# Kernel optimization log

Hardware: AMD Instinct MI355X
Metric: run time of the kernel (lower is better)

The kernel has to match this reference:

```python
import jax, jax.numpy as jnp
import numpy as np

N_NODES = 100000
N_EDGES = 800000
IN_DIM, HID, OUT_DIM = 128, 96, 32
BN_EPS = 1e-5


def gcn_conv(x, W, b, src, dst, n):
    # PyG GCNConv: linear -> symmetric-normalized aggregation (with self-loops) -> +bias
    h = x @ W  # [N, out]
    sl = jnp.arange(n)
    s = jnp.concatenate([src, sl])
    d = jnp.concatenate([dst, sl])
    deg = jax.ops.segment_sum(jnp.ones(s.shape[0], dtype=x.dtype), d, num_segments=n)
    dinv = jnp.where(deg > 0, jax.lax.rsqrt(deg), 0.0)
    norm = dinv[s] * dinv[d]  # [E+N]
    out = jax.ops.segment_sum(norm[:, None] * h[s], d, num_segments=n)
    return out + b


def batchnorm(x, gamma, beta):
    mu = jnp.mean(x, axis=0)
    var = jnp.var(x, axis=0)
    return gamma * (x - mu) * jax.lax.rsqrt(var + BN_EPS) + beta


def setup_inputs() -> dict:
    key = jax.random.key(0)
    ks = jax.random.split(key, 8)
    glorot = lambda k, fi, fo: jax.random.normal(k, (fi, fo), jnp.float32) * np.sqrt(2.0 / (fi + fo))
    return {
        "x": jax.random.normal(ks[0], (N_NODES, IN_DIM), jnp.float32),
        "edge_index": jax.random.randint(ks[1], (2, N_EDGES), 0, N_NODES, jnp.int64),
        "W1": glorot(ks[2], IN_DIM, HID), "b1": jnp.zeros((HID,), jnp.float32),
        "W2": glorot(ks[3], HID, HID), "b2": jnp.zeros((HID,), jnp.float32),
        "W3": glorot(ks[4], HID, OUT_DIM), "b3": jnp.zeros((OUT_DIM,), jnp.float32),
        "g1": jnp.ones((HID,), jnp.float32), "be1": jnp.zeros((HID,), jnp.float32),
        "g2": jnp.ones((HID,), jnp.float32), "be2": jnp.zeros((HID,), jnp.float32),
    }


def reference(x, edge_index, W1, b1, W2, b2, W3, b3, g1, be1, g2, be2):
    src, dst = edge_index[0], edge_index[1]
    n = x.shape[0]
    h = gcn_conv(x, W1, b1, src, dst, n)
    h = jax.nn.relu(batchnorm(h, g1, be1))  # dropout is identity in eval
    h = gcn_conv(h, W2, b2, src, dst, n)
    h = jax.nn.relu(batchnorm(h, g2, be2))
    h = gcn_conv(h, W3, b3, src, dst, n)
    return jax.nn.log_softmax(h, axis=-1)
```

## Files before the change

kernel.cpp:

```cpp
#include <hip/hip_runtime.h>
#include <hip/hip_fp16.h>
#include <cstddef>

#define NN 100000
#define NE 800000
#define DIN 128
#define HID 96
#define DOUT 32
static constexpr float BN_EPS = 1e-5f;
#define SCAN_NB ((NN + 255) / 256)

typedef unsigned short u16;
typedef unsigned int u32;

__device__ __forceinline__ float b2f(u32 lo16) {
    union { u32 u; float f; } c; c.u = lo16 << 16; return c.f;
}
__device__ __forceinline__ u16 f2b(float f) {
    union { float f; u32 u; } c; c.f = f;
    return (u16)((c.u + 0x7FFFu + ((c.u >> 16) & 1u)) >> 16);
}
__device__ __forceinline__ u32 pack_edge(int s, float w) {
    __half h = __float2half(w);
    return ((u32)s << 15) | (u32)__half_as_ushort(h);
}
__device__ __forceinline__ int edge_src(u32 pk) { return (int)(pk >> 15); }
__device__ __forceinline__ float edge_wt(u32 pk) {
    return __half2float(__ushort_as_half((u16)(pk & 0x7FFFu)));
}


__global__ void k_init(int* __restrict__ deg) {
    int i = blockIdx.x * 256 + threadIdx.x;
    if (i < NN) deg[i] = 0;
}

__global__ __launch_bounds__(256) void k_scan1(const int* __restrict__ deg,
                                               int* __restrict__ row_start,
                                               int* __restrict__ blksum,
                                               float* __restrict__ dinv) {
    __shared__ int lds[256];
    int t = threadIdx.x;
    int i = blockIdx.x * 256 + t;
    int v = (i < NN) ? deg[i] : 0;
    if (i < NN) dinv[i] = rsqrtf((float)(v + 1));
    lds[t] = v;
    __syncthreads();
#pragma unroll
    for (int off = 1; off < 256; off <<= 1) {
        int add = (t >= off) ? lds[t - off] : 0;
        __syncthreads();
        lds[t] += add;
        __syncthreads();
    }
    if (i < NN) row_start[i] = lds[t] - v;
    if (t == 255) blksum[blockIdx.x] = lds[255];
}

__global__ __launch_bounds__(512) void k_scan2(int* __restrict__ blksum,
                                               int* __restrict__ row_start,
                                               float* __restrict__ meta) {
    __shared__ int lds[512];
    int t = threadIdx.x;
    if (t < 384) meta[t] = 0.f;
    int v = (t < SCAN_NB) ? blksum[t] : 0;
    lds[t] = v;
    __syncthreads();
#pragma unroll
    for (int off = 1; off < 512; off <<= 1) {
        int add = (t >= off) ? lds[t - off] : 0;
        __syncthreads();
        lds[t] += add;
        __syncthreads();
    }
    if (t < SCAN_NB) blksum[t] = lds[t] - v;
    if (t == 511) row_start[NN] = lds[511];
}

__global__ __launch_bounds__(256) void k_scan3(int* __restrict__ row_start,
                                               const int* __restrict__ blksum) {
    int i = blockIdx.x * 256 + threadIdx.x;
    if (i < NN) row_start[i] += blksum[blockIdx.x];
}

__global__ void k_scatter(const int* __restrict__ src, const int* __restrict__ dst,
                          const int* __restrict__ row_start,
                          const int* __restrict__ rank,
                          const float* __restrict__ dinv,
                          u32* __restrict__ ewt) {
    int e = blockIdx.x * blockDim.x + threadIdx.x;
    if (e < NE) {
        int d = dst[e];
        int p = row_start[d] + rank[e];
        int s = src[e];
        ewt[p] = pack_edge(s, dinv[s]);
    }
}

template <int KD, int ND, bool FUSE, typename XT>
__device__ __forceinline__ void gemm_body(int bid, const XT* __restrict__ X,
                                          const float* __restrict__ W,
                                          u16* __restrict__ Z,
                                          const float* __restrict__ bnA,
                                          const float* __restrict__ bnC, int M) {
    constexpr int BK = 32;
    constexpr int CT = 16;
    constexpr int CPT = ND / CT;
    constexpr int RPT = 8;
    constexpr int XS = 132;
    __shared__ float Xs[BK * XS];
    __shared__ float Ws[BK * ND];
    __shared__ float As[KD], Cs[KD];

    int tid = threadIdx.x;
    if (FUSE && tid < KD) { As[tid] = bnA[tid]; Cs[tid] = bnC[tid]; }
    int row0 = bid * 128;
    int ct = tid % CT, rt = tid / CT;
    float acc[RPT][CPT];
#pragma unroll
    for (int r = 0; r < RPT; ++r)
#pragma unroll
        for (int c = 0; c < CPT; ++c) acc[r][c] = 0.f;

    for (int k0 = 0; k0 < KD; k0 += BK) {
        __syncthreads();
        if constexpr (sizeof(XT) == 4) {
#pragma unroll
            for (int pass = 0; pass < 4; ++pass) {
                int r = pass * 32 + (tid >> 3);
                int kq = (tid & 7) * 4;
                int grow = row0 + r;
                float4 v = make_float4(0.f, 0.f, 0.f, 0.f);
                if (grow < M) v = *(const float4*)&X[(size_t)grow * KD + k0 + kq];
                if (FUSE) {
                    v.x = fmaxf(fmaf(As[k0 + kq + 0], v.x, Cs[k0 + kq + 0]), 0.f);
                    v.y = fmaxf(fmaf(As[k0 + kq + 1], v.y, Cs[k0 + kq + 1]), 0.f);
                    v.z = fmaxf(fmaf(As[k0 + kq + 2], v.z, Cs[k0 + kq + 2]), 0.f);
                    v.w = fmaxf(fmaf(As[k0 + kq + 3], v.w, Cs[k0 + kq + 3]), 0.f);
                }
                Xs[(kq + 0) * XS + r] = v.x;
                Xs[(kq + 1) * XS + r] = v.y;
                Xs[(kq + 2) * XS + r] = v.z;
                Xs[(kq + 3) * XS + r] = v.w;
            }
        } else {
#pragma unroll
            for (int pass = 0; pass < 2; ++pass) {
                int r = pass * 64 + (tid >> 2);
                int kq = (tid & 3) * 8;
                int grow = row0 + r;
                uint4 v = make_uint4(0, 0, 0, 0);
                if (grow < M) v = *(const uint4*)&X[(size_t)grow * KD + k0 + kq];
                u32 w[4] = {v.x, v.y, v.z, v.w};
#pragma unroll
                for (int q = 0; q < 4; ++q) {
                    float lo = b2f(w[q] & 0xFFFFu);
                    float hi = b2f(w[q] >> 16);
                    if (FUSE) {
                        lo = fmaxf(fmaf(As[k0 + kq + 2 * q + 0], lo, Cs[k0 + kq + 2 * q + 0]), 0.f);
                        hi = fmaxf(fmaf(As[k0 + kq + 2 * q + 1], hi, Cs[k0 + kq + 2 * q + 1]), 0.f);
                    }
                    Xs[(kq + 2 * q + 0) * XS + r] = lo;
                    Xs[(kq + 2 * q + 1) * XS + r] = hi;
                }
            }
        }
#pragma unroll
        for (int f = tid; f < BK * ND / 4; f += 256) {
            int kk = f / (ND / 4);
            int c4 = (f % (ND / 4)) * 4;
            *(float4*)&Ws[kk * ND + c4] = *(const float4*)&W[(size_t)(k0 + kk) * ND + c4];
        }
        __syncthreads();
#pragma unroll
        for (int kk = 0; kk < BK; ++kk) {
            float4 x0 = *(const float4*)&Xs[kk * XS + rt * 8];
            float4 x1 = *(const float4*)&Xs[kk * XS + rt * 8 + 4];
            float xr[RPT] = {x0.x, x0.y, x0.z, x0.w, x1.x, x1.y, x1.z, x1.w};
            float wc[CPT];
#pragma unroll
            for (int c = 0; c < CPT; ++c) wc[c] = Ws[kk * ND + ct * CPT + c];
#pragma unroll
            for (int r = 0; r < RPT; ++r)
#pragma unroll
                for (int c = 0; c < CPT; ++c) acc[r][c] = fmaf(xr[r], wc[c], acc[r][c]);
        }
    }
#pragma unroll
    for (int r = 0; r < RPT; ++r) {
        int grow = row0 + rt * RPT + r;
        if (grow < M) {
#pragma unroll
            for (int c = 0; c < CPT; c += 2) {
                u32 pk = (u32)f2b(acc[r][c]) | ((u32)f2b(acc[r][c + 1]) << 16);
                *(u32*)&Z[(size_t)grow * ND + ct * CPT + c] = pk;
            }
        }
    }
}

template <int KD, int ND, bool FUSE, typename XT>
__global__ __launch_bounds__(256) void k_gemm(const XT* __restrict__ X,
                                              const float* __restrict__ W,
                                              u16* __restrict__ Z,
                                              const float* __restrict__ bnA,
                                              const float* __restrict__ bnC, int M) {
    gemm_body<KD, ND, FUSE, XT>(blockIdx.x, X, W, Z, bnA, bnC, M);
}

__global__ __launch_bounds__(256) void k_gemm1_hist(const float* __restrict__ X,
                                                    const float* __restrict__ W,
                                                    u16* __restrict__ Z, int M,
                                                    int gemm_blocks,
                                                    const int* __restrict__ dst,
                                                    int* __restrict__ deg,
                                                    int* __restrict__ rank) {
    if ((int)blockIdx.x < gemm_blocks) {
        gemm_body<DIN, HID, false, float>(blockIdx.x, X, W, Z, nullptr, nullptr, M);
    } else {
        int e = ((int)blockIdx.x - gemm_blocks) * 256 + (int)threadIdx.x;
        if (e < NE) rank[e] = atomicAdd(&deg[dst[e]], 1);
    }
}

#define ACC8(UB, W)                                                     \
    acc[0] = fmaf(W, b2f((UB).x & 0xFFFFu), acc[0]);                    \
    acc[1] = fmaf(W, b2f((UB).x >> 16), acc[1]);                        \
    acc[2] = fmaf(W, b2f((UB).y & 0xFFFFu), acc[2]);                    \
    acc[3] = fmaf(W, b2f((UB).y >> 16), acc[3]);                        \
    acc[4] = fmaf(W, b2f((UB).z & 0xFFFFu), acc[4]);                    \
    acc[5] = fmaf(W, b2f((UB).z >> 16), acc[5]);                        \
    acc[6] = fmaf(W, b2f((UB).w & 0xFFFFu), acc[6]);                    \
    acc[7] = fmaf(W, b2f((UB).w >> 16), acc[7]);

__global__ __launch_bounds__(256) void k_agg96(const u16* __restrict__ Z,
                                               u16* __restrict__ H,
                                               const float* __restrict__ bias,
                                               const int* __restrict__ row_start,
                                               const u32* __restrict__ ewt,
                                               const float* __restrict__ dinv,
                                               float* __restrict__ gsum,
                                               float* __restrict__ gsq) {
    __shared__ float ssum[96], ssq[96];
    int tid = threadIdx.x;
    if (tid < 96) { ssum[tid] = 0.f; ssq[tid] = 0.f; }
    __syncthreads();
    int wid = tid >> 6, lane = tid & 63;
    int r = lane >> 4;
    int jraw = lane & 15;
    int j = jraw < 12 ? jraw : 11;
    bool jact = jraw < 12;
    u32 j16 = (u32)j << 4;
    const char* zb = (const char*)Z;
    float bia[8];
#pragma unroll
    for (int k = 0; k < 8; ++k) bia[k] = bias[8 * j + k];
    float lsum[8], lsq[8];
#pragma unroll
    for (int k = 0; k < 8; ++k) { lsum[k] = 0.f; lsq[k] = 0.f; }
    const int S = gridDim.x * 4;

    int n = blockIdx.x * 4 + wid;
    int e0 = 0, e1 = 0;
    u32 pr = 0;
    if (n < NN) {
        e0 = row_start[n]; e1 = row_start[n + 1];
        if (e0 + lane < e1) pr = ewt[e0 + lane];
    }
    while (n < NN) {
        int n2 = n + S;
        int e0n = 0, e1n = 0;
        if (n2 < NN) { e0n = row_start[n2]; e1n = row_start[n2 + 1]; }
        u32 prn = 0;
        if (n2 < NN && e0n + lane < e1n) prn = ewt[e0n + lane];

        float dn = dinv[n];
        int m = e1 - e0;
        float acc[8];
        uint4 us4 = make_uint4(0, 0, 0, 0);
        if (r == 0) us4 = *(const uint4*)(zb + (u32)n * 192u + j16);
        if (r == 0) {
            acc[0] = dn * b2f(us4.x & 0xFFFFu); acc[1] = dn * b2f(us4.x >> 16);
            acc[2] = dn * b2f(us4.y & 0xFFFFu); acc[3] = dn * b2f(us4.y >> 16);
            acc[4] = dn * b2f(us4.z & 0xFFFFu); acc[5] = dn * b2f(us4.z >> 16);
            acc[6] = dn * b2f(us4.w & 0xFFFFu); acc[7] = dn * b2f(us4.w >> 16);
        } else {
#pragma unroll
            for (int k = 0; k < 8; ++k) acc[k] = 0.f;
        }

        if (m <= 16) {
            uint4 ub[4]; float wc[4];
            int nch = (m + 3) >> 2;
#pragma unroll
            for (int c = 0; c < 4; ++c) {
                if (c < nch) {
                    int e = 4 * c + r;
                    u32 pk = __shfl(pr, e < m ? e : 0);
                    wc[c] = (e < m) ? edge_wt(pk) : 0.f;
                    ub[c] = *(const uint4*)(zb + (pk >> 15) * 192u + j16);
                }
            }
#pragma unroll
            for (int c = 0; c < 4; ++c) {
                if (c < nch) { ACC8(ub[c], wc[c]); }
            }
        } else {
            for (int base = 0; base < m; base += 64) {
                u32 cw = pr;
                if (base) {
                    int idx = e0 + base + lane;
                    cw = (idx < e1) ? ewt[idx] : 0;
                }
                int lim = m - base; if (lim > 64) lim = 64;
                for (int c = 0; c < lim; c += 4) {
                    int e = c + r;
                    u32 pk = __shfl(cw, e < lim ? e : 0);
                    float w = (e < lim) ? edge_wt(pk) : 0.f;
                    uint4 ub = *(const uint4*)(zb + (pk >> 15) * 192u + j16);
                    ACC8(ub, w);
                }
            }
        }

#pragma unroll
        for (int k = 0; k < 8; ++k) {
            float v = acc[k];
            v += __shfl_xor(v, 16);
            v += __shfl_xor(v, 32);
            acc[k] = v;
        }
        if (r == 0 && jact) {
            float h[8];
#pragma unroll
            for (int k = 0; k < 8; ++k) {
                h[k] = fmaf(dn, acc[k], bia[k]);
                lsum[k] += h[k];
                lsq[k] = fmaf(h[k], h[k], lsq[k]);
            }
            uint4 o;
            o.x = (u32)f2b(h[0]) | ((u32)f2b(h[1]) << 16);
            o.y = (u32)f2b(h[2]) | ((u32)f2b(h[3]) << 16);
            o.z = (u32)f2b(h[4]) | ((u32)f2b(h[5]) << 16);
            o.w = (u32)f2b(h[6]) | ((u32)f2b(h[7]) << 16);
            *(uint4*)((char*)H + (u32)n * 192u + j16) = o;
        }
        n = n2; e0 = e0n; e1 = e1n; pr = prn;
    }
    if (r == 0 && jact) {
#pragma unroll
        for (int k = 0; k < 8; ++k) {
            atomicAdd(&ssum[8 * j + k], lsum[k]);
            atomicAdd(&ssq[8 * j + k], lsq[k]);
        }
    }
    __syncthreads();
    if (tid < 96) { atomicAdd(&gsum[tid], ssum[tid]); atomicAdd(&gsq[tid], ssq[tid]); }
}

__global__ void k_bncoef(const float* __restrict__ gsum, const float* __restrict__ gsq,
                         const float* __restrict__ g, const float* __restrict__ be,
                         float* __restrict__ bnA, float* __restrict__ bnC) {
    int c = threadIdx.x;
    if (c < 96) {
        float mean = gsum[c] * (1.f / NN);
        float var = gsq[c] * (1.f / NN) - mean * mean;
        float inv = rsqrtf(var + BN_EPS);
        float a = g[c] * inv;
        bnA[c] = a;
        bnC[c] = fmaf(-a, mean, be[c]);
    }
}

__global__ __launch_bounds__(256) void k_agg32_lsm(const u16* __restrict__ Z,
                                                   float* __restrict__ Out,
                                                   const float* __restrict__ bias,
                                                   const int* __restrict__ row_start,
                                                   const u32* __restrict__ ewt,
                                                   const float* __restrict__ dinv) {
    int tid = threadIdx.x;
    int wid = tid >> 6, lane = tid & 63;
    int g = lane >> 4, sl = lane & 15;
    const u32* zu = (const u32*)Z;
    float b0 = bias[2 * sl], b1 = bias[2 * sl + 1];
    int stride = gridDim.x * 16;
    for (int n0 = (blockIdx.x * 4 + wid) * 4; n0 < NN; n0 += stride) {
        int n = n0 + g;
        bool vn = n < NN;
        float dn = vn ? dinv[n] : 0.f;
        u32 uself = vn ? zu[(size_t)n * 16 + sl] : 0;
        float a0a = dn * b2f(uself & 0xFFFFu);
        float a1a = dn * b2f(uself >> 16);
        float a0b = 0.f, a1b = 0.f;
        int e0 = vn ? row_start[n] : 0, e1 = vn ? row_start[n + 1] : 0;
        for (int eb = e0; eb < e1; eb += 16) {
            int m = e1 - eb; if (m > 16) m = 16;
            int idx = eb + sl;
            u32 plv = (idx < e1) ? ewt[idx] : 0;
            u32 u_[16]; float w_[16];
#pragma unroll
            for (int q = 0; q < 16; ++q) {
                bool v = q < m;
                u32 pk = __shfl(plv, v ? q : 0, 16);
                w_[q] = v ? edge_wt(pk) : 0.f;
                u_[q] = zu[(size_t)edge_src(pk) * 16 + sl];
            }
#pragma unroll
            for (int q = 0; q < 16; q += 2) {
                a0a = fmaf(w_[q], b2f(u_[q] & 0xFFFFu), a0a);
                a1a = fmaf(w_[q], b2f(u_[q] >> 16), a1a);
                a0b = fmaf(w_[q + 1], b2f(u_[q + 1] & 0xFFFFu), a0b);
                a1b = fmaf(w_[q + 1], b2f(u_[q + 1] >> 16), a1b);
            }
        }
        float v0 = fmaf(dn, a0a + a0b, b0);
        float v1 = fmaf(dn, a1a + a1b, b1);
        float mx = fmaxf(v0, v1);
#pragma unroll
        for (int off = 8; off; off >>= 1) mx = fmaxf(mx, __shfl_xor(mx, off, 16));
        float ex = __expf(v0 - mx) + __expf(v1 - mx);
#pragma unroll
        for (int off = 8; off; off >>= 1) ex += __shfl_xor(ex, off, 16);
        float lse = mx + __logf(ex);
        if (vn) {
            float2 o = make_float2(v0 - lse, v1 - lse);
            *(float2*)&Out[(size_t)n * 32 + 2 * sl] = o;
        }
    }
}


extern "C" void kernel_launch(void* const* d_in, const int* in_sizes, int n_in,
                              void* d_out, int out_size, void* d_ws, size_t ws_size,
                              hipStream_t stream) {
    const float* x  = (const float*)d_in[0];
    const int* ei   = (const int*)d_in[1];
    const float* W1 = (const float*)d_in[2];
    const float* b1 = (const float*)d_in[3];
    const float* W2 = (const float*)d_in[4];
    const float* b2 = (const float*)d_in[5];
    const float* W3 = (const float*)d_in[6];
    const float* b3 = (const float*)d_in[7];
    const float* g1 = (const float*)d_in[8];
    const float* be1 = (const float*)d_in[9];
    const float* g2 = (const float*)d_in[10];
    const float* be2 = (const float*)d_in[11];
    float* out = (float*)d_out;

    const int* src = ei;
    const int* dst = ei + NE;

    char* p = (char*)d_ws;
    size_t off = 0;
    auto take = [&](size_t bytes) {
        char* r = p + off;
        off = (off + bytes + 255) & ~(size_t)255;
        return r;
    };
    float* dinv      = (float*)take(NN * 4);
    int*   deg       = (int*)take(NN * 4);
    int*   row_start = (int*)take((NN + 1) * 4);
    int*   blksum    = (int*)take(SCAN_NB * 4);
    int*   rank      = (int*)take((size_t)NE * 4);
    u32*   ewt       = (u32*)take((size_t)NE * 4);
    float* meta      = (float*)take(768 * 4);
    u16*   bufA      = (u16*)take((size_t)NN * HID * 2);
    u16*   bufB      = (u16*)take((size_t)NN * HID * 2);

    float* sum1 = meta + 0,   *sq1 = meta + 96;
    float* sum2 = meta + 192, *sq2 = meta + 288;
    float* bnA1 = meta + 384, *bnC1 = meta + 480;
    float* bnA2 = meta + 576, *bnC2 = meta + 672;

    const int EB = (NE + 255) / 256;
    const int VB = (NN + 255) / 256;
    const int GB = (NN + 127) / 128;
    const int AB = 2048;

    k_init<<<VB, 256, 0, stream>>>(deg);
    k_gemm1_hist<<<GB + EB, 256, 0, stream>>>(x, W1, bufA, NN, GB, dst, deg, rank);
    k_scan1<<<SCAN_NB, 256, 0, stream>>>(deg, row_start, blksum, dinv);
    k_scan2<<<1, 512, 0, stream>>>(blksum, row_start, meta);
    k_scan3<<<SCAN_NB, 256, 0, stream>>>(row_start, blksum);
    k_scatter<<<EB, 256, 0, stream>>>(src, dst, row_start, rank, dinv, ewt);

    k_agg96<<<AB, 256, 0, stream>>>(bufA, bufB, b1, row_start, ewt, dinv, sum1, sq1);
    k_bncoef<<<1, 128, 0, stream>>>(sum1, sq1, g1, be1, bnA1, bnC1);

    k_gemm<HID, HID, true, u16><<<GB, 256, 0, stream>>>(bufB, W2, bufA, bnA1, bnC1, NN);
    k_agg96<<<AB, 256, 0, stream>>>(bufA, bufB, b2, row_start, ewt, dinv, sum2, sq2);
    k_bncoef<<<1, 128, 0, stream>>>(sum2, sq2, g2, be2, bnA2, bnC2);

    k_gemm<HID, DOUT, true, u16><<<GB, 256, 0, stream>>>(bufB, W3, bufA, bnA2, bnC2, NN);
    k_agg32_lsm<<<AB, 256, 0, stream>>>(bufA, out, b3, row_start, ewt, dinv);

    (void)in_sizes; (void)n_in; (void)out_size; (void)ws_size;
}
```

Before: 422.6 us.

## Move dense GEMMs to bf16x3 split MFMA with prepacked weight fragments

Replaces the scalar FP32 register-tiled GEMMs with MFMA 16x16x32 bf16 instructions. Each operand is split into hi/lo bf16 parts and three products are summed to keep near-FP32 accuracy. A new kernel packs the weights once per call into the MFMA fragment layout. Tiles shrink to 64 rows with the whole K dimension staged in LDS. The aim is to cut GEMM compute time, at the cost of an extra launch, extra conversion ALU work and 3x the MFMA count.

```diff
diff --git a/kernel.cpp b/kernel.cpp
--- a/kernel.cpp
+++ b/kernel.cpp
@@ -13,6 +13,9 @@
 typedef unsigned short u16;
 typedef unsigned int u32;
 
+using f32x4 = __attribute__((ext_vector_type(4))) float;
+using bf16x8 = __attribute__((ext_vector_type(8))) short;
+
 __device__ __forceinline__ float b2f(u32 lo16) {
     union { u32 u; float f; } c; c.u = lo16 << 16; return c.f;
 }
@@ -33,6 +36,30 @@
 __global__ void k_init(int* __restrict__ deg) {
     int i = blockIdx.x * 256 + threadIdx.x;
     if (i < NN) deg[i] = 0;
+}
+
+__global__ __launch_bounds__(256) void k_wpack(const float* __restrict__ W1,
+                                               const float* __restrict__ W2,
+                                               const float* __restrict__ W3,
+                                               u16* __restrict__ w1p,
+                                               u16* __restrict__ w2p,
+                                               u16* __restrict__ w3p) {
+    int e = blockIdx.x * 256 + threadIdx.x;
+    const float* W; u16* P; int N, nf, idx;
+    if (e < 12288)      { W = W1; P = w1p; N = 96; nf = 24; idx = e; }
+    else if (e < 21504) { W = W2; P = w2p; N = 96; nf = 18; idx = e - 12288; }
+    else                { W = W3; P = w3p; N = 32; nf = 6;  idx = e - 21504; }
+    int f = idx >> 9, r = idx & 511;
+    int lane = r >> 3, j = r & 7;
+    int CFT = N / 16;
+    int kt = f / CFT, c = f % CFT;
+    int k = kt * 32 + (lane >> 4) * 8 + j;
+    int col = c * 16 + (lane & 15);
+    float v = W[k * N + col];
+    u16 hi = f2b(v);
+    u16 lo = f2b(v - b2f(hi));
+    P[idx] = hi;
+    P[nf * 512 + idx] = lo;
 }
 
 __global__ __launch_bounds__(256) void k_scan1(const int* __restrict__ deg,
@@ -97,126 +124,141 @@
     }
 }
 
-template <int KD, int ND, bool FUSE, typename XT>
-__device__ __forceinline__ void gemm_body(int bid, const XT* __restrict__ X,
-                                          const float* __restrict__ W,
-                                          u16* __restrict__ Z,
-                                          const float* __restrict__ bnA,
-                                          const float* __restrict__ bnC, int M) {
-    constexpr int BK = 32;
-    constexpr int CT = 16;
-    constexpr int CPT = ND / CT;
-    constexpr int RPT = 8;
-    constexpr int XS = 132;
-    __shared__ float Xs[BK * XS];
-    __shared__ float Ws[BK * ND];
-    __shared__ float As[KD], Cs[KD];
+template <int K, int N, bool FUSE, typename XT>
+__device__ __forceinline__ void gemmM_body(int bid, const XT* __restrict__ X,
+                                           const u16* __restrict__ Wp,
+                                           u16* __restrict__ Z,
+                                           const float* __restrict__ bnA,
+                                           const float* __restrict__ bnC, int M) {
+    constexpr int KT = K / 32;
+    constexpr int CFT = N / 16;
+    constexpr int WN = (N == 96) ? 2 : 1;
+    constexpr int WM = 4 / WN;
+    constexpr int CF = CFT / WN;
+    constexpr int RF = 64 / (WM * 16);
+    constexpr int XSB = K + 8;
+    __shared__ u16 Ah[64 * XSB];
+    __shared__ u16 Al[64 * XSB];
+    __shared__ float As[FUSE ? K : 1], Cs[FUSE ? K : 1];
 
     int tid = threadIdx.x;
-    if (FUSE && tid < KD) { As[tid] = bnA[tid]; Cs[tid] = bnC[tid]; }
-    int row0 = bid * 128;
-    int ct = tid % CT, rt = tid / CT;
-    float acc[RPT][CPT];
-#pragma unroll
-    for (int r = 0; r < RPT; ++r)
-#pragma unroll
-        for (int c = 0; c < CPT; ++c) acc[r][c] = 0.f;
-
-    for (int k0 = 0; k0 < KD; k0 += BK) {
+    if (FUSE) {
+        if (tid < K) { As[tid] = bnA[tid]; Cs[tid] = bnC[tid]; }
         __syncthreads();
-        if constexpr (sizeof(XT) == 4) {
-#pragma unroll
-            for (int pass = 0; pass < 4; ++pass) {
-                int r = pass * 32 + (tid >> 3);
-                int kq = (tid & 7) * 4;
-                int grow = row0 + r;
-                float4 v = make_float4(0.f, 0.f, 0.f, 0.f);
-                if (grow < M) v = *(const float4*)&X[(size_t)grow * KD + k0 + kq];
+    }
+    int row0 = bid * 64;
+    int sr = tid >> 2, sq = tid & 3;
+    int grow = row0 + sr;
+    if constexpr (sizeof(XT) == 4) {
+#pragma unroll
+        for (int i = 0; i < 8; ++i) {
+            int c0 = sq * 32 + i * 4;
+            float4 v = make_float4(0.f, 0.f, 0.f, 0.f);
+            if (grow < M) v = *(const float4*)&X[(size_t)grow * K + c0];
+            float vv[4] = {v.x, v.y, v.z, v.w};
+            u32 hpk[2], lpk[2];
+#pragma unroll
+            for (int p = 0; p < 2; ++p) {
+                u16 h0 = f2b(vv[2 * p]), h1 = f2b(vv[2 * p + 1]);
+                u16 l0 = f2b(vv[2 * p] - b2f(h0));
+                u16 l1 = f2b(vv[2 * p + 1] - b2f(h1));
+                hpk[p] = (u32)h0 | ((u32)h1 << 16);
+                lpk[p] = (u32)l0 | ((u32)l1 << 16);
+            }
+            *(uint2*)&Ah[sr * XSB + c0] = make_uint2(hpk[0], hpk[1]);
+            *(uint2*)&Al[sr * XSB + c0] = make_uint2(lpk[0], lpk[1]);
+        }
+    } else {
+#pragma unroll
+        for (int i = 0; i < 3; ++i) {
+            int c0 = sq * 24 + i * 8;
+            uint4 v = make_uint4(0, 0, 0, 0);
+            if (grow < M) v = *(const uint4*)&X[(size_t)grow * K + c0];
+            u32 w[4] = {v.x, v.y, v.z, v.w};
+            u32 hq[4], lq[4];
+#pragma unroll
+            for (int p = 0; p < 4; ++p) {
+                float x0 = b2f(w[p] & 0xFFFFu);
+                float x1 = b2f(w[p] >> 16);
                 if (FUSE) {
-                    v.x = fmaxf(fmaf(As[k0 + kq + 0], v.x, Cs[k0 + kq + 0]), 0.f);
-                    v.y = fmaxf(fmaf(As[k0 + kq + 1], v.y, Cs[k0 + kq + 1]), 0.f);
-                    v.z = fmaxf(fmaf(As[k0 + kq + 2], v.z, Cs[k0 + kq + 2]), 0.f);
-                    v.w = fmaxf(fmaf(As[k0 + kq + 3], v.w, Cs[k0 + kq + 3]), 0.f);
+                    x0 = fmaxf(fmaf(As[c0 + 2 * p], x0, Cs[c0 + 2 * p]), 0.f);
+                    x1 = fmaxf(fmaf(As[c0 + 2 * p + 1], x1, Cs[c0 + 2 * p + 1]), 0.f);
                 }
-                Xs[(kq + 0) * XS + r] = v.x;
-                Xs[(kq + 1) * XS + r] = v.y;
-                Xs[(kq + 2) * XS + r] = v.z;
-                Xs[(kq + 3) * XS + r] = v.w;
-            }
-        } else {
-#pragma unroll
-            for (int pass = 0; pass < 2; ++pass) {
-                int r = pass * 64 + (tid >> 2);
-                int kq = (tid & 3) * 8;
-                int grow = row0 + r;
-                uint4 v = make_uint4(0, 0, 0, 0);
-                if (grow < M) v = *(const uint4*)&X[(size_t)grow * KD + k0 + kq];
-                u32 w[4] = {v.x, v.y, v.z, v.w};
-#pragma unroll
-                for (int q = 0; q < 4; ++q) {
-                    float lo = b2f(w[q] & 0xFFFFu);
-                    float hi = b2f(w[q] >> 16);
-                    if (FUSE) {
-                        lo = fmaxf(fmaf(As[k0 + kq + 2 * q + 0], lo, Cs[k0 + kq + 2 * q + 0]), 0.f);
-                        hi = fmaxf(fmaf(As[k0 + kq + 2 * q + 1], hi, Cs[k0 + kq + 2 * q + 1]), 0.f);
-                    }
-                    Xs[(kq + 2 * q + 0) * XS + r] = lo;
-                    Xs[(kq + 2 * q + 1) * XS + r] = hi;
+                u16 h0 = f2b(x0), h1 = f2b(x1);
+                u16 l0 = f2b(x0 - b2f(h0)), l1 = f2b(x1 - b2f(h1));
+                hq[p] = (u32)h0 | ((u32)h1 << 16);
+                lq[p] = (u32)l0 | ((u32)l1 << 16);
+            }
+            *(uint4*)&Ah[sr * XSB + c0] = make_uint4(hq[0], hq[1], hq[2], hq[3]);
+            *(uint4*)&Al[sr * XSB + c0] = make_uint4(lq[0], lq[1], lq[2], lq[3]);
+        }
+    }
+    __syncthreads();
+
+    int wid = tid >> 6, lane = tid & 63;
+    int wm = wid & (WM - 1), wn = wid / WM;
+    int lr = lane & 15, lg = lane >> 4;
+    f32x4 acc[RF][CF];
+#pragma unroll
+    for (int a = 0; a < RF; ++a)
+#pragma unroll
+        for (int b = 0; b < CF; ++b) acc[a][b] = (f32x4){0.f, 0.f, 0.f, 0.f};
+
+    const u16* WpLo = Wp + KT * CFT * 512;
+#pragma unroll
+    for (int kt = 0; kt < KT; ++kt) {
+        bf16x8 ah[RF], al[RF];
+#pragma unroll
+        for (int rf = 0; rf < RF; ++rf) {
+            int row = wm * (RF * 16) + rf * 16 + lr;
+            ah[rf] = *(const bf16x8*)&Ah[row * XSB + kt * 32 + lg * 8];
+            al[rf] = *(const bf16x8*)&Al[row * XSB + kt * 32 + lg * 8];
+        }
+#pragma unroll
+        for (int cf = 0; cf < CF; ++cf) {
+            int f = kt * CFT + wn * CF + cf;
+            bf16x8 bh = *(const bf16x8*)&Wp[f * 512 + lane * 8];
+            bf16x8 bl = *(const bf16x8*)&WpLo[f * 512 + lane * 8];
+#pragma unroll
+            for (int rf = 0; rf < RF; ++rf) {
+                acc[rf][cf] = __builtin_amdgcn_mfma_f32_16x16x32_bf16(ah[rf], bh, acc[rf][cf], 0, 0, 0);
+                acc[rf][cf] = __builtin_amdgcn_mfma_f32_16x16x32_bf16(al[rf], bh, acc[rf][cf], 0, 0, 0);
+                acc[rf][cf] = __builtin_amdgcn_mfma_f32_16x16x32_bf16(ah[rf], bl, acc[rf][cf], 0, 0, 0);
+            }
+        }
+    }
+#pragma unroll
+    for (int rf = 0; rf < RF; ++rf)
+#pragma unroll
+        for (int cf = 0; cf < CF; ++cf)
+#pragma unroll
+            for (int rr = 0; rr < 4; ++rr) {
+                int gr = row0 + wm * (RF * 16) + rf * 16 + lg * 4 + rr;
+                if (gr < M) {
+                    int col = (wn * CF + cf) * 16 + lr;
+                    Z[(size_t)gr * N + col] = f2b(acc[rf][cf][rr]);
                 }
             }
-        }
-#pragma unroll
-        for (int f = tid; f < BK * ND / 4; f += 256) {
-            int kk = f / (ND / 4);
-            int c4 = (f % (ND / 4)) * 4;
-            *(float4*)&Ws[kk * ND + c4] = *(const float4*)&W[(size_t)(k0 + kk) * ND + c4];
-        }
-        __syncthreads();
-#pragma unroll
-        for (int kk = 0; kk < BK; ++kk) {
-            float4 x0 = *(const float4*)&Xs[kk * XS + rt * 8];
-            float4 x1 = *(const float4*)&Xs[kk * XS + rt * 8 + 4];
-            float xr[RPT] = {x0.x, x0.y, x0.z, x0.w, x1.x, x1.y, x1.z, x1.w};
-            float wc[CPT];
-#pragma unroll
-            for (int c = 0; c < CPT; ++c) wc[c] = Ws[kk * ND + ct * CPT + c];
-#pragma unroll
-            for (int r = 0; r < RPT; ++r)
-#pragma unroll
-                for (int c = 0; c < CPT; ++c) acc[r][c] = fmaf(xr[r], wc[c], acc[r][c]);
-        }
-    }
-#pragma unroll
-    for (int r = 0; r < RPT; ++r) {
-        int grow = row0 + rt * RPT + r;
-        if (grow < M) {
-#pragma unroll
-            for (int c = 0; c < CPT; c += 2) {
-                u32 pk = (u32)f2b(acc[r][c]) | ((u32)f2b(acc[r][c + 1]) << 16);
-                *(u32*)&Z[(size_t)grow * ND + ct * CPT + c] = pk;
-            }
-        }
-    }
-}
-
-template <int KD, int ND, bool FUSE, typename XT>
+}
+
+template <int K, int N, bool FUSE, typename XT>
 __global__ __launch_bounds__(256) void k_gemm(const XT* __restrict__ X,
-                                              const float* __restrict__ W,
+                                              const u16* __restrict__ Wp,
                                               u16* __restrict__ Z,
                                               const float* __restrict__ bnA,
                                               const float* __restrict__ bnC, int M) {
-    gemm_body<KD, ND, FUSE, XT>(blockIdx.x, X, W, Z, bnA, bnC, M);
+    gemmM_body<K, N, FUSE, XT>(blockIdx.x, X, Wp, Z, bnA, bnC, M);
 }
 
 __global__ __launch_bounds__(256) void k_gemm1_hist(const float* __restrict__ X,
-                                                    const float* __restrict__ W,
+                                                    const u16* __restrict__ Wp,
                                                     u16* __restrict__ Z, int M,
                                                     int gemm_blocks,
                                                     const int* __restrict__ dst,
                                                     int* __restrict__ deg,
                                                     int* __restrict__ rank) {
     if ((int)blockIdx.x < gemm_blocks) {
-        gemm_body<DIN, HID, false, float>(blockIdx.x, X, W, Z, nullptr, nullptr, M);
+        gemmM_body<DIN, HID, false, float>(blockIdx.x, X, Wp, Z, nullptr, nullptr, M);
     } else {
         int e = ((int)blockIdx.x - gemm_blocks) * 256 + (int)threadIdx.x;
         if (e < NE) rank[e] = atomicAdd(&deg[dst[e]], 1);
@@ -464,6 +506,9 @@
     int*   rank      = (int*)take((size_t)NE * 4);
     u32*   ewt       = (u32*)take((size_t)NE * 4);
     float* meta      = (float*)take(768 * 4);
+    u16*   w1p       = (u16*)take(24 * 512 * 2 * 2);
+    u16*   w2p       = (u16*)take(18 * 512 * 2 * 2);
+    u16*   w3p       = (u16*)take(6 * 512 * 2 * 2);
     u16*   bufA      = (u16*)take((size_t)NN * HID * 2);
     u16*   bufB      = (u16*)take((size_t)NN * HID * 2);
 
@@ -474,11 +519,12 @@
 
     const int EB = (NE + 255) / 256;
     const int VB = (NN + 255) / 256;
-    const int GB = (NN + 127) / 128;
+    const int MB = (NN + 63) / 64;
     const int AB = 2048;
 
+    k_wpack<<<96, 256, 0, stream>>>(W1, W2, W3, w1p, w2p, w3p);
     k_init<<<VB, 256, 0, stream>>>(deg);
-    k_gemm1_hist<<<GB + EB, 256, 0, stream>>>(x, W1, bufA, NN, GB, dst, deg, rank);
+    k_gemm1_hist<<<MB + EB, 256, 0, stream>>>(x, w1p, bufA, NN, MB, dst, deg, rank);
     k_scan1<<<SCAN_NB, 256, 0, stream>>>(deg, row_start, blksum, dinv);
     k_scan2<<<1, 512, 0, stream>>>(blksum, row_start, meta);
     k_scan3<<<SCAN_NB, 256, 0, stream>>>(row_start, blksum);
@@ -487,11 +533,11 @@
     k_agg96<<<AB, 256, 0, stream>>>(bufA, bufB, b1, row_start, ewt, dinv, sum1, sq1);
     k_bncoef<<<1, 128, 0, stream>>>(sum1, sq1, g1, be1, bnA1, bnC1);
 
-    k_gemm<HID, HID, true, u16><<<GB, 256, 0, stream>>>(bufB, W2, bufA, bnA1, bnC1, NN);
+    k_gemm<HID, HID, true, u16><<<MB, 256, 0, stream>>>(bufB, w2p, bufA, bnA1, bnC1, NN);
     k_agg96<<<AB, 256, 0, stream>>>(bufA, bufB, b2, row_start, ewt, dinv, sum2, sq2);
     k_bncoef<<<1, 128, 0, stream>>>(sum2, sq2, g2, be2, bnA2, bnC2);
 
-    k_gemm<HID, DOUT, true, u16><<<GB, 256, 0, stream>>>(bufB, W3, bufA, bnA2, bnC2, NN);
+    k_gemm<HID, DOUT, true, u16><<<MB, 256, 0, stream>>>(bufB, w3p, bufA, bnA2, bnC2, NN);
     k_agg32_lsm<<<AB, 256, 0, stream>>>(bufA, out, b3, row_start, ewt, dinv);
 
     (void)in_sizes; (void)n_in; (void)out_size; (void)ws_size;
```

New measurement: 384.6 us. 1.1x faster.
